# Optimization experiments

Measured on AMD Instinct MI355X. Metric: run time of the kernel, lower is better.

## Reference

```python
import jax, jax.numpy as jnp
import numpy as np

N, IN_DIM, HID = 8192, 256, 128


def _glorot(key, shape):
    lim = float(np.sqrt(6.0 / (shape[0] + shape[1])))
    return jax.random.uniform(key, shape, jnp.float32, -lim, lim)


def setup_inputs() -> dict:
    key = jax.random.key(0)
    ks = jax.random.split(key, 16)
    return {
        "x": jax.random.normal(ks[0], (N, IN_DIM), jnp.float32),
        "XY_Adj": jnp.zeros((N, N), jnp.float32),  # unused: overwritten by Cos_Adj in forward
        "w0": _glorot(ks[1], (IN_DIM, HID)),
        "w1": _glorot(ks[2], (IN_DIM, HID)),
        "Wq1": _glorot(ks[3], (IN_DIM, HID)), "bq1": jnp.zeros((HID,), jnp.float32),
        "Wk1": _glorot(ks[4], (IN_DIM, HID)), "bk1": jnp.zeros((HID,), jnp.float32),
        "Wv1": _glorot(ks[5], (IN_DIM, HID)), "bv1": jnp.zeros((HID,), jnp.float32),
        "Ws1": _glorot(ks[6], (IN_DIM, HID)), "bs1": jnp.zeros((HID,), jnp.float32),
        "Wq4": _glorot(ks[7], (HID, IN_DIM)), "bq4": jnp.zeros((IN_DIM,), jnp.float32),
        "Wk4": _glorot(ks[8], (HID, IN_DIM)), "bk4": jnp.zeros((IN_DIM,), jnp.float32),
        "Wv4": _glorot(ks[9], (HID, IN_DIM)), "bv4": jnp.zeros((IN_DIM,), jnp.float32),
        "Ws4": _glorot(ks[10], (HID, IN_DIM)), "bs4": jnp.zeros((IN_DIM,), jnp.float32),
    }


def _cos_adj(x, w0, w1):
    # Dense cosine-similarity adjacency, as in Cos_Adj.forward
    theta = x @ w0  # [N, HID]
    phi = x @ w1    # [N, HID]
    tn = jnp.linalg.norm(theta, axis=1, keepdims=True)  # [N,1]
    pn = jnp.linalg.norm(phi, axis=1, keepdims=True)    # [N,1]
    return (theta @ phi.T) / (tn @ pn.T + 1e-20)        # [N,N]


def _tconv(h, Wq, bq, Wk, bk, Wv, bv, Ws, bs):
    # PyG TransformerConv (heads=1, root_weight=True) on the fully-connected
    # graph produced by coo_matrix(sim_graph) == dense all-pairs attention.
    q = h @ Wq + bq
    k = h @ Wk + bk
    v = h @ Wv + bv
    scale = 1.0 / np.sqrt(q.shape[-1])
    attn = jax.nn.softmax((q @ k.T) * scale, axis=-1)  # [N,N]
    return attn @ v + (h @ Ws + bs)


def reference(x, XY_Adj, w0, w1,
              Wq1, bq1, Wk1, bk1, Wv1, bv1, Ws1, bs1,
              Wq4, bq4, Wk4, bk4, Wv4, bv4, Ws4, bs4):
    # Adjacency values only define the edge set (all N^2 pairs nonzero for
    # generic inputs); TransformerConv recomputes attention coefficients.
    sim = _cos_adj(x, w0, w1)  # noqa: F841 (edge set = nonzeros = all pairs)
    h1 = jax.nn.elu(_tconv(x, Wq1, bq1, Wk1, bk1, Wv1, bv1, Ws1, bs1))
    out = _tconv(h1, Wq4, bq4, Wk4, bk4, Wv4, bv4, Ws4, bs4)
    return out
```

## Files before the change

### kernel.cpp

```cpp
#include <hip/hip_runtime.h>

#define N_ROWS 8192
#define IN_DIM 256
#define HID 128

typedef __attribute__((ext_vector_type(8))) short bf16x8;
typedef __attribute__((ext_vector_type(4))) float f32x4;

__device__ __forceinline__ unsigned short f2bf(float f) {
    union { float f; unsigned u; } v; v.f = f;
    unsigned r = (v.u + 0x7FFFu + ((v.u >> 16) & 1u)) >> 16;
    return (unsigned short)r;
}

__device__ __forceinline__ unsigned cvt_pk_bf16(float lo, float hi) {
    unsigned r;
    asm("v_cvt_pk_bf16_f32 %0, %1, %2" : "=v"(r) : "v"(lo), "v"(hi));
    return r;
}

__global__ void pack_weights(const float* __restrict__ W0, const float* __restrict__ W1,
                             const float* __restrict__ W2, const float* __restrict__ W3,
                             const float* __restrict__ b0, const float* __restrict__ b1,
                             const float* __restrict__ b2, const float* __restrict__ b3,
                             unsigned short* __restrict__ WT, float* __restrict__ B,
                             int K, int HO)
{
    int NT = 4 * HO;
    int idx = blockIdx.x * blockDim.x + threadIdx.x;
    if (idx < NT * K) {
        int n = idx / K, k = idx - n * K;
        int s = n / HO, sn = n - s * HO;
        const float* W = (s == 0) ? W0 : (s == 1) ? W1 : (s == 2) ? W2 : W3;
        WT[idx] = f2bf(W[k * HO + sn]);
    }
    if (idx < NT) {
        int s = idx / HO, sn = idx - s * HO;
        const float* b = (s == 0) ? b0 : (s == 1) ? b1 : (s == 2) ? b2 : b3;
        B[idx] = b[sn];
    }
}

__global__ void cast_x(const float* __restrict__ in, unsigned short* __restrict__ out, int n) {
    int i = blockIdx.x * blockDim.x + threadIdx.x;
    if (i < n) out[i] = f2bf(in[i]);
}

__global__ void transpose_bf16(const unsigned short* __restrict__ in,
                               unsigned short* __restrict__ out, int R, int C)
{
    __shared__ unsigned short t[32][33];
    const int tx = threadIdx.x, ty = threadIdx.y;
    const int r0 = blockIdx.y * 32, c0 = blockIdx.x * 32;
    #pragma unroll
    for (int j = 0; j < 32; j += 8)
        t[ty + j][tx] = in[(size_t)(r0 + ty + j) * C + c0 + tx];
    __syncthreads();
    #pragma unroll
    for (int j = 0; j < 32; j += 8)
        out[(size_t)(c0 + ty + j) * R + r0 + tx] = t[tx][ty + j];
}

template<int K>
__global__ __launch_bounds__(256) void proj_gemm(
    const unsigned short* __restrict__ A, const unsigned short* __restrict__ WT,
    const float* __restrict__ bias,
    unsigned short* __restrict__ qo, unsigned short* __restrict__ ko,
    unsigned short* __restrict__ vo, float* __restrict__ skip,
    int NT, float qScale)
{
    const int lane = threadIdx.x & 63;
    const int wid = (blockIdx.x * blockDim.x + threadIdx.x) >> 6;
    const int nStrips = NT / 64;
    const int mTile = wid / nStrips;
    const int nBase = (wid - mTile * nStrips) * 64;
    const int l15 = lane & 15, lg = lane >> 4;
    const int HO = NT >> 2;

    f32x4 acc[4];
    #pragma unroll
    for (int c = 0; c < 4; ++c) acc[c] = f32x4{0.f, 0.f, 0.f, 0.f};

    const unsigned short* Ap = A + (size_t)(mTile * 16 + l15) * K + lg * 8;
    #pragma unroll
    for (int t = 0; t < K / 32; ++t) {
        bf16x8 a = *(const bf16x8*)(Ap + t * 32);
        #pragma unroll
        for (int c = 0; c < 4; ++c) {
            bf16x8 b = *(const bf16x8*)(WT + (size_t)(nBase + c * 16 + l15) * K + t * 32 + lg * 8);
            acc[c] = __builtin_amdgcn_mfma_f32_16x16x32_bf16(a, b, acc[c], 0, 0, 0);
        }
    }
    #pragma unroll
    for (int c = 0; c < 4; ++c) {
        int col = nBase + c * 16 + l15;
        int sec = col / HO, sc = col - sec * HO;
        float bv = bias[col];
        #pragma unroll
        for (int r = 0; r < 4; ++r) {
            int mrow = mTile * 16 + lg * 4 + r;
            float val = acc[c][r] + bv;
            size_t o = (size_t)mrow * HO + sc;
            if (sec == 0) qo[o] = f2bf(val * qScale);
            else if (sec == 1) ko[o] = f2bf(val);
            else if (sec == 2) vo[o] = f2bf(val);
            else skip[o] = val;
        }
    }
}

template<int D, int KB>
__global__ __launch_bounds__(512) void attn_partial(
    const unsigned short* __restrict__ Qm,
    const unsigned short* __restrict__ Km,
    const unsigned short* __restrict__ VTg,
    float* __restrict__ accOut, float* __restrict__ mOut, float* __restrict__ lOut,
    int chunkLen)
{
    constexpr int TPB = 512;
    constexpr int LK = D + 8;
    constexpr int LV = KB + 8;
    constexpr int DT = D / 16;
    constexpr int CT = KB / 16;
    constexpr int KS = KB / 32;
    static_assert(KB * D / 8 / TPB == 2, "two K staging int4s per thread");
    static_assert(D * KB / 8 / TPB == 2, "two V staging int4s per thread");
    __shared__ __align__(16) unsigned short Kl[KB * LK];
    __shared__ __align__(16) unsigned short VTl[D * LV];

    const int tid = threadIdx.x;
    const int lane = tid & 63;
    const int w = tid >> 6;
    const int l15 = lane & 15, lg = lane >> 4;
    const int qrow = blockIdx.x * 128 + w * 16;
    const int kStart = blockIdx.y * chunkLen;
    const size_t NN = N_ROWS;

    const int kr0 = tid / (D / 8), kc0 = tid - kr0 * (D / 8);
    const int kr1 = (tid + TPB) / (D / 8), kc1 = (tid + TPB) - kr1 * (D / 8);
    const int kg0 = kr0 * D + kc0 * 8, kl0 = kr0 * LK + kc0 * 8;
    const int kg1 = kr1 * D + kc1 * 8, kl1 = kr1 * LK + kc1 * 8;
    const int vr0 = tid / (KB / 8), vc0 = tid - vr0 * (KB / 8);
    const int vr1 = (tid + TPB) / (KB / 8), vc1 = (tid + TPB) - vr1 * (KB / 8);
    const int vg0 = vr0 * (int)NN + vc0 * 8, vl0 = vr0 * LV + vc0 * 8;
    const int vg1 = vr1 * (int)NN + vc1 * 8, vl1 = vr1 * LV + vc1 * 8;

    bf16x8 qf[D / 32];
    #pragma unroll
    for (int t = 0; t < D / 32; ++t)
        qf[t] = *(const bf16x8*)(Qm + (size_t)(qrow + l15) * D + t * 32 + lg * 8);

    f32x4 acc[DT];
    #pragma unroll
    for (int dt = 0; dt < DT; ++dt) acc[dt] = f32x4{0.f, 0.f, 0.f, 0.f};
    float mReg = -__builtin_inff();
    float lReg = 0.f;

    const int nt = chunkLen / KB;
    const unsigned short* Kp = Km + (size_t)kStart * D;
    const unsigned short* Vp = VTg + kStart;
    int4 pk0 = *(const int4*)(Kp + kg0);
    int4 pk1 = *(const int4*)(Kp + kg1);
    int4 pv0 = *(const int4*)(Vp + vg0);
    int4 pv1 = *(const int4*)(Vp + vg1);

    for (int t = 0; t < nt; ++t) {
        __syncthreads();
        *(int4*)(&Kl[kl0]) = pk0;
        *(int4*)(&Kl[kl1]) = pk1;
        *(int4*)(&VTl[vl0]) = pv0;
        *(int4*)(&VTl[vl1]) = pv1;
        __syncthreads();
        if (t + 1 < nt) {
            const unsigned short* KpN = Kp + (size_t)(t + 1) * KB * D;
            const unsigned short* VpN = Vp + (t + 1) * KB;
            pk0 = *(const int4*)(KpN + kg0);
            pk1 = *(const int4*)(KpN + kg1);
            pv0 = *(const int4*)(VpN + vg0);
            pv1 = *(const int4*)(VpN + vg1);
        }
        f32x4 sT[CT];
        __builtin_amdgcn_s_setprio(1);
        #pragma unroll
        for (int c = 0; c < CT; ++c) {
            sT[c] = f32x4{0.f, 0.f, 0.f, 0.f};
            #pragma unroll
            for (int tt = 0; tt < D / 32; ++tt) {
                bf16x8 kf = *(const bf16x8*)(&Kl[(c * 16 + l15) * LK + tt * 32 + lg * 8]);
                sT[c] = __builtin_amdgcn_mfma_f32_16x16x32_bf16(kf, qf[tt], sT[c], 0, 0, 0);
            }
        }
        __builtin_amdgcn_s_setprio(0);
        float pmax = sT[0][0];
        #pragma unroll
        for (int c = 0; c < CT; ++c)
            #pragma unroll
            for (int r = 0; r < 4; ++r) pmax = fmaxf(pmax, sT[c][r]);
        bool need = pmax > mReg + 8.f;
        if (__any(need)) {
            float v = pmax;
            v = fmaxf(v, __shfl_xor(v, 16));
            v = fmaxf(v, __shfl_xor(v, 32));
            float mN = fmaxf(mReg, v);
            float al = exp2f(mReg - mN);
            mReg = mN;
            lReg *= al;
            #pragma unroll
            for (int dt = 0; dt < DT; ++dt) acc[dt] *= al;
        }
        unsigned Wp[CT][2];
        float lsum = 0.f;
        #pragma unroll
        for (int c = 0; c < CT; ++c) {
            float p0 = exp2f(sT[c][0] - mReg);
            float p1 = exp2f(sT[c][1] - mReg);
            float p2 = exp2f(sT[c][2] - mReg);
            float p3 = exp2f(sT[c][3] - mReg);
            lsum += (p0 + p1) + (p2 + p3);
            Wp[c][0] = cvt_pk_bf16(p0, p1);
            Wp[c][1] = cvt_pk_bf16(p2, p3);
        }
        lReg += lsum;
        #pragma unroll
        for (int ks = 0; ks < KS; ++ks) {
            unsigned x0 = Wp[2 * ks][0], x1 = Wp[2 * ks][1];
            unsigned x2 = Wp[2 * ks + 1][0], x3 = Wp[2 * ks + 1][1];
            const bool g1 = (lg & 2) != 0, g0 = (lg & 1) != 0;
            unsigned s0 = g1 ? x0 : x2, s1 = g1 ? x1 : x3;
            unsigned r0 = __shfl_xor(s0, 32), r1 = __shfl_xor(s1, 32);
            unsigned k0 = g1 ? x2 : x0, k1 = g1 ? x3 : x1;
            unsigned t0 = (g0 != g1) ? k0 : r0, t1 = (g0 != g1) ? k1 : r1;
            unsigned q0 = __shfl_xor(t0, 16), q1 = __shfl_xor(t1, 16);
            union { unsigned u[4]; bf16x8 v; } pb;
            pb.u[0] = g0 ? q0 : (g1 ? r0 : k0);
            pb.u[1] = g0 ? q1 : (g1 ? r1 : k1);
            pb.u[2] = g0 ? (g1 ? k0 : r0) : q0;
            pb.u[3] = g0 ? (g1 ? k1 : r1) : q1;
            __builtin_amdgcn_s_setprio(1);
            #pragma unroll
            for (int dt = 0; dt < DT; ++dt) {
                bf16x8 va = *(const bf16x8*)(&VTl[(dt * 16 + l15) * LV + ks * 32 + lg * 8]);
                acc[dt] = __builtin_amdgcn_mfma_f32_16x16x32_bf16(va, pb.v, acc[dt], 0, 0, 0);
            }
            __builtin_amdgcn_s_setprio(0);
        }
    }

    lReg += __shfl_xor(lReg, 16);
    lReg += __shfl_xor(lReg, 32);

    float* accRow = accOut + ((size_t)blockIdx.y * NN + qrow + l15) * D + lg * 4;
    #pragma unroll
    for (int dt = 0; dt < DT; ++dt)
        *(f32x4*)(accRow + dt * 16) = acc[dt];
    if (lg == 0) {
        mOut[blockIdx.y * NN + qrow + l15] = mReg;
        lOut[blockIdx.y * NN + qrow + l15] = lReg;
    }
}

template<int D, bool ELU>
__global__ void combine_kernel(const float* __restrict__ acc, const float* __restrict__ mArr,
                               const float* __restrict__ lArr, const float* __restrict__ skip,
                               float* __restrict__ outF, unsigned short* __restrict__ outB,
                               int CH)
{
    const int row = blockIdx.x;
    const int d = threadIdx.x;
    const size_t NN = N_ROWS;
    float mStar = -__builtin_inff();
    for (int c = 0; c < CH; ++c) mStar = fmaxf(mStar, mArr[c * NN + row]);
    float denom = 0.f, val = 0.f;
    for (int c = 0; c < CH; ++c) {
        float wgt = exp2f(mArr[c * NN + row] - mStar);
        denom += wgt * lArr[c * NN + row];
        val += wgt * acc[((size_t)c * NN + row) * D + d];
    }
    float v = val / denom + skip[(size_t)row * D + d];
    if (ELU) {
        v = (v > 0.f) ? v : expm1f(v);
        outB[(size_t)row * D + d] = f2bf(v);
    } else {
        outF[(size_t)row * D + d] = v;
    }
}

extern "C" void kernel_launch(void* const* d_in, const int* in_sizes, int n_in,
                              void* d_out, int out_size, void* d_ws, size_t ws_size,
                              hipStream_t stream)
{
    (void)in_sizes; (void)n_in; (void)out_size;
    const float* x   = (const float*)d_in[0];
    const float* Wq1 = (const float*)d_in[4];
    const float* bq1 = (const float*)d_in[5];
    const float* Wk1 = (const float*)d_in[6];
    const float* bk1 = (const float*)d_in[7];
    const float* Wv1 = (const float*)d_in[8];
    const float* bv1 = (const float*)d_in[9];
    const float* Ws1 = (const float*)d_in[10];
    const float* bs1 = (const float*)d_in[11];
    const float* Wq4 = (const float*)d_in[12];
    const float* bq4 = (const float*)d_in[13];
    const float* Wk4 = (const float*)d_in[14];
    const float* bk4 = (const float*)d_in[15];
    const float* Wv4 = (const float*)d_in[16];
    const float* bv4 = (const float*)d_in[17];
    const float* Ws4 = (const float*)d_in[18];
    const float* bs4 = (const float*)d_in[19];
    float* out = (float*)d_out;

    const int N = N_ROWS;
    size_t off = 0;
    auto alloc = [&](size_t bytes) -> void* {
        void* p = (char*)d_ws + off;
        off = (off + bytes + 255) & ~(size_t)255;
        return p;
    };
    unsigned short* xb  = (unsigned short*)alloc((size_t)N * IN_DIM * 2);
    unsigned short* WT1 = (unsigned short*)alloc((size_t)512 * 256 * 2);
    float* B1           = (float*)alloc(512 * 4);
    unsigned short* WT4 = (unsigned short*)alloc((size_t)1024 * 128 * 2);
    float* B4           = (float*)alloc(1024 * 4);
    unsigned short* q1  = (unsigned short*)alloc((size_t)N * HID * 2);
    unsigned short* k1  = (unsigned short*)alloc((size_t)N * HID * 2);
    unsigned short* v1  = (unsigned short*)alloc((size_t)N * HID * 2);
    unsigned short* VT1g= (unsigned short*)alloc((size_t)HID * N * 2);
    float* skip1        = (float*)alloc((size_t)N * HID * 4);
    unsigned short* h1  = (unsigned short*)alloc((size_t)N * HID * 2);
    unsigned short* q4  = (unsigned short*)alloc((size_t)N * IN_DIM * 2);
    unsigned short* k4  = (unsigned short*)alloc((size_t)N * IN_DIM * 2);
    unsigned short* v4  = (unsigned short*)alloc((size_t)N * IN_DIM * 2);
    unsigned short* VT4g= (unsigned short*)alloc((size_t)IN_DIM * N * 2);
    float* skip4        = (float*)alloc((size_t)N * IN_DIM * 4);

    size_t fixedEnd = off;
    size_t perCH = (size_t)N * 4 * 4 + (size_t)N * HID * 4 + (size_t)N * IN_DIM * 4 + 4096;
    int CH = 8;
    while (CH > 1 && fixedEnd + (size_t)CH * perCH > ws_size) CH >>= 1;

    float* m1   = (float*)alloc((size_t)CH * N * 4);
    float* l1   = (float*)alloc((size_t)CH * N * 4);
    float* m2   = (float*)alloc((size_t)CH * N * 4);
    float* l2   = (float*)alloc((size_t)CH * N * 4);
    float* acc1 = (float*)alloc((size_t)CH * N * HID * 4);
    float* acc2 = (float*)alloc((size_t)CH * N * IN_DIM * 4);
    if (off > ws_size && CH == 1) acc2 = out;

    const float LOG2E = 1.4426950408889634f;
    const float qs1 = 0.088388347648318447f * LOG2E;
    const float qs2 = 0.0625f * LOG2E;

    pack_weights<<<dim3((512 * 256 + 255) / 256), dim3(256), 0, stream>>>(
        Wq1, Wk1, Wv1, Ws1, bq1, bk1, bv1, bs1, WT1, B1, 256, 128);
    pack_weights<<<dim3((1024 * 128 + 255) / 256), dim3(256), 0, stream>>>(
        Wq4, Wk4, Wv4, Ws4, bq4, bk4, bv4, bs4, WT4, B4, 128, 256);
    cast_x<<<dim3((N * IN_DIM + 255) / 256), dim3(256), 0, stream>>>(x, xb, N * IN_DIM);

    proj_gemm<256><<<dim3((N / 16) * (512 / 64) / 4), dim3(256), 0, stream>>>(
        xb, WT1, B1, q1, k1, v1, skip1, 512, qs1);
    transpose_bf16<<<dim3(HID / 32, N / 32), dim3(32, 8), 0, stream>>>(v1, VT1g, N, HID);
    attn_partial<128, 64><<<dim3(N / 128, CH), dim3(512), 0, stream>>>(
        q1, k1, VT1g, acc1, m1, l1, N / CH);
    combine_kernel<128, true><<<dim3(N), dim3(128), 0, stream>>>(
        acc1, m1, l1, skip1, (float*)nullptr, h1, CH);

    proj_gemm<128><<<dim3((N / 16) * (1024 / 64) / 4), dim3(256), 0, stream>>>(
        h1, WT4, B4, q4, k4, v4, skip4, 1024, qs2);
    transpose_bf16<<<dim3(IN_DIM / 32, N / 32), dim3(32, 8), 0, stream>>>(v4, VT4g, N, IN_DIM);
    attn_partial<256, 32><<<dim3(N / 128, CH), dim3(512), 0, stream>>>(
        q4, k4, VT4g, acc2, m2, l2, N / CH);
    combine_kernel<256, false><<<dim3(N), dim3(256), 0, stream>>>(
        acc2, m2, l2, skip4, out, (unsigned short*)nullptr, CH);
}
```

Baseline: 277.9 us.

## Process two 16-row query tiles per wave in attention to reuse K/V LDS fragments

Each wave now handles 32 query rows (two 16-row MFMA tiles) instead of 16. Every K and V fragment read from LDS is reused across both query tiles, which halves LDS reads and K/V global staging per query row. The grid is halved to match. In exchange, register pressure roughly doubles for the accumulators, which matters most for D=256, and there are fewer blocks to fill the GPU, especially if CH is small.

```diff
diff --git a/kernel.cpp b/kernel.cpp
--- a/kernel.cpp
+++ b/kernel.cpp
@@ -109,7 +109,7 @@
     }
 }
 
-template<int D, int KB>
+template<int D, int KB, int Q2>
 __global__ __launch_bounds__(512) void attn_partial(
     const unsigned short* __restrict__ Qm,
     const unsigned short* __restrict__ Km,
@@ -123,6 +123,7 @@
     constexpr int DT = D / 16;
     constexpr int CT = KB / 16;
     constexpr int KS = KB / 32;
+    constexpr int QW = 16 * Q2;
     static_assert(KB * D / 8 / TPB == 2, "two K staging int4s per thread");
     static_assert(D * KB / 8 / TPB == 2, "two V staging int4s per thread");
     __shared__ __align__(16) unsigned short Kl[KB * LK];
@@ -132,7 +133,7 @@
     const int lane = tid & 63;
     const int w = tid >> 6;
     const int l15 = lane & 15, lg = lane >> 4;
-    const int qrow = blockIdx.x * 128 + w * 16;
+    const int qrow = blockIdx.x * (8 * QW) + w * QW;
     const int kStart = blockIdx.y * chunkLen;
     const size_t NN = N_ROWS;
 
@@ -145,16 +146,22 @@
     const int vg0 = vr0 * (int)NN + vc0 * 8, vl0 = vr0 * LV + vc0 * 8;
     const int vg1 = vr1 * (int)NN + vc1 * 8, vl1 = vr1 * LV + vc1 * 8;
 
-    bf16x8 qf[D / 32];
-    #pragma unroll
-    for (int t = 0; t < D / 32; ++t)
-        qf[t] = *(const bf16x8*)(Qm + (size_t)(qrow + l15) * D + t * 32 + lg * 8);
-
-    f32x4 acc[DT];
-    #pragma unroll
-    for (int dt = 0; dt < DT; ++dt) acc[dt] = f32x4{0.f, 0.f, 0.f, 0.f};
-    float mReg = -__builtin_inff();
-    float lReg = 0.f;
+    bf16x8 qf[Q2][D / 32];
+    #pragma unroll
+    for (int m = 0; m < Q2; ++m)
+        #pragma unroll
+        for (int t = 0; t < D / 32; ++t)
+            qf[m][t] = *(const bf16x8*)(Qm + (size_t)(qrow + m * 16 + l15) * D + t * 32 + lg * 8);
+
+    f32x4 acc[Q2][DT];
+    float mReg[Q2], lReg[Q2];
+    #pragma unroll
+    for (int m = 0; m < Q2; ++m) {
+        #pragma unroll
+        for (int dt = 0; dt < DT; ++dt) acc[m][dt] = f32x4{0.f, 0.f, 0.f, 0.f};
+        mReg[m] = -__builtin_inff();
+        lReg[m] = 0.f;
+    }
 
     const int nt = chunkLen / KB;
     const unsigned short* Kp = Km + (size_t)kStart * D;
@@ -179,83 +186,108 @@
             pv0 = *(const int4*)(VpN + vg0);
             pv1 = *(const int4*)(VpN + vg1);
         }
-        f32x4 sT[CT];
+        f32x4 sT[Q2][CT];
         __builtin_amdgcn_s_setprio(1);
         #pragma unroll
         for (int c = 0; c < CT; ++c) {
-            sT[c] = f32x4{0.f, 0.f, 0.f, 0.f};
+            #pragma unroll
+            for (int m = 0; m < Q2; ++m) sT[m][c] = f32x4{0.f, 0.f, 0.f, 0.f};
             #pragma unroll
             for (int tt = 0; tt < D / 32; ++tt) {
                 bf16x8 kf = *(const bf16x8*)(&Kl[(c * 16 + l15) * LK + tt * 32 + lg * 8]);
-                sT[c] = __builtin_amdgcn_mfma_f32_16x16x32_bf16(kf, qf[tt], sT[c], 0, 0, 0);
+                #pragma unroll
+                for (int m = 0; m < Q2; ++m)
+                    sT[m][c] = __builtin_amdgcn_mfma_f32_16x16x32_bf16(kf, qf[m][tt], sT[m][c], 0, 0, 0);
             }
         }
         __builtin_amdgcn_s_setprio(0);
-        float pmax = sT[0][0];
-        #pragma unroll
-        for (int c = 0; c < CT; ++c)
-            #pragma unroll
-            for (int r = 0; r < 4; ++r) pmax = fmaxf(pmax, sT[c][r]);
-        bool need = pmax > mReg + 8.f;
+        float pmax[Q2];
+        bool need = false;
+        #pragma unroll
+        for (int m = 0; m < Q2; ++m) {
+            float v = sT[m][0][0];
+            #pragma unroll
+            for (int c = 0; c < CT; ++c)
+                #pragma unroll
+                for (int r = 0; r < 4; ++r) v = fmaxf(v, sT[m][c][r]);
+            pmax[m] = v;
+            need = need || (v > mReg[m] + 8.f);
+        }
         if (__any(need)) {
-            float v = pmax;
-            v = fmaxf(v, __shfl_xor(v, 16));
-            v = fmaxf(v, __shfl_xor(v, 32));
-            float mN = fmaxf(mReg, v);
-            float al = exp2f(mReg - mN);
-            mReg = mN;
-            lReg *= al;
-            #pragma unroll
-            for (int dt = 0; dt < DT; ++dt) acc[dt] *= al;
-        }
-        unsigned Wp[CT][2];
-        float lsum = 0.f;
-        #pragma unroll
-        for (int c = 0; c < CT; ++c) {
-            float p0 = exp2f(sT[c][0] - mReg);
-            float p1 = exp2f(sT[c][1] - mReg);
-            float p2 = exp2f(sT[c][2] - mReg);
-            float p3 = exp2f(sT[c][3] - mReg);
-            lsum += (p0 + p1) + (p2 + p3);
-            Wp[c][0] = cvt_pk_bf16(p0, p1);
-            Wp[c][1] = cvt_pk_bf16(p2, p3);
-        }
-        lReg += lsum;
+            #pragma unroll
+            for (int m = 0; m < Q2; ++m) {
+                float v = pmax[m];
+                v = fmaxf(v, __shfl_xor(v, 16));
+                v = fmaxf(v, __shfl_xor(v, 32));
+                float mN = fmaxf(mReg[m], v);
+                float al = exp2f(mReg[m] - mN);
+                mReg[m] = mN;
+                lReg[m] *= al;
+                #pragma unroll
+                for (int dt = 0; dt < DT; ++dt) acc[m][dt] *= al;
+            }
+        }
+        unsigned Wp[Q2][CT][2];
+        #pragma unroll
+        for (int m = 0; m < Q2; ++m) {
+            float lsum = 0.f;
+            #pragma unroll
+            for (int c = 0; c < CT; ++c) {
+                float p0 = exp2f(sT[m][c][0] - mReg[m]);
+                float p1 = exp2f(sT[m][c][1] - mReg[m]);
+                float p2 = exp2f(sT[m][c][2] - mReg[m]);
+                float p3 = exp2f(sT[m][c][3] - mReg[m]);
+                lsum += (p0 + p1) + (p2 + p3);
+                Wp[m][c][0] = cvt_pk_bf16(p0, p1);
+                Wp[m][c][1] = cvt_pk_bf16(p2, p3);
+            }
+            lReg[m] += lsum;
+        }
         #pragma unroll
         for (int ks = 0; ks < KS; ++ks) {
-            unsigned x0 = Wp[2 * ks][0], x1 = Wp[2 * ks][1];
-            unsigned x2 = Wp[2 * ks + 1][0], x3 = Wp[2 * ks + 1][1];
-            const bool g1 = (lg & 2) != 0, g0 = (lg & 1) != 0;
-            unsigned s0 = g1 ? x0 : x2, s1 = g1 ? x1 : x3;
-            unsigned r0 = __shfl_xor(s0, 32), r1 = __shfl_xor(s1, 32);
-            unsigned k0 = g1 ? x2 : x0, k1 = g1 ? x3 : x1;
-            unsigned t0 = (g0 != g1) ? k0 : r0, t1 = (g0 != g1) ? k1 : r1;
-            unsigned q0 = __shfl_xor(t0, 16), q1 = __shfl_xor(t1, 16);
-            union { unsigned u[4]; bf16x8 v; } pb;
-            pb.u[0] = g0 ? q0 : (g1 ? r0 : k0);
-            pb.u[1] = g0 ? q1 : (g1 ? r1 : k1);
-            pb.u[2] = g0 ? (g1 ? k0 : r0) : q0;
-            pb.u[3] = g0 ? (g1 ? k1 : r1) : q1;
+            bf16x8 pbv[Q2];
+            #pragma unroll
+            for (int m = 0; m < Q2; ++m) {
+                unsigned x0 = Wp[m][2 * ks][0], x1 = Wp[m][2 * ks][1];
+                unsigned x2 = Wp[m][2 * ks + 1][0], x3 = Wp[m][2 * ks + 1][1];
+                const bool g1 = (lg & 2) != 0, g0 = (lg & 1) != 0;
+                unsigned s0 = g1 ? x0 : x2, s1 = g1 ? x1 : x3;
+                unsigned r0 = __shfl_xor(s0, 32), r1 = __shfl_xor(s1, 32);
+                unsigned k0 = g1 ? x2 : x0, k1 = g1 ? x3 : x1;
+                unsigned t0 = (g0 != g1) ? k0 : r0, t1 = (g0 != g1) ? k1 : r1;
+                unsigned q0 = __shfl_xor(t0, 16), q1 = __shfl_xor(t1, 16);
+                union { unsigned u[4]; bf16x8 v; } pb;
+                pb.u[0] = g0 ? q0 : (g1 ? r0 : k0);
+                pb.u[1] = g0 ? q1 : (g1 ? r1 : k1);
+                pb.u[2] = g0 ? (g1 ? k0 : r0) : q0;
+                pb.u[3] = g0 ? (g1 ? k1 : r1) : q1;
+                pbv[m] = pb.v;
+            }
             __builtin_amdgcn_s_setprio(1);
             #pragma unroll
             for (int dt = 0; dt < DT; ++dt) {
                 bf16x8 va = *(const bf16x8*)(&VTl[(dt * 16 + l15) * LV + ks * 32 + lg * 8]);
-                acc[dt] = __builtin_amdgcn_mfma_f32_16x16x32_bf16(va, pb.v, acc[dt], 0, 0, 0);
+                #pragma unroll
+                for (int m = 0; m < Q2; ++m)
+                    acc[m][dt] = __builtin_amdgcn_mfma_f32_16x16x32_bf16(va, pbv[m], acc[m][dt], 0, 0, 0);
             }
             __builtin_amdgcn_s_setprio(0);
         }
     }
 
-    lReg += __shfl_xor(lReg, 16);
-    lReg += __shfl_xor(lReg, 32);
-
-    float* accRow = accOut + ((size_t)blockIdx.y * NN + qrow + l15) * D + lg * 4;
-    #pragma unroll
-    for (int dt = 0; dt < DT; ++dt)
-        *(f32x4*)(accRow + dt * 16) = acc[dt];
-    if (lg == 0) {
-        mOut[blockIdx.y * NN + qrow + l15] = mReg;
-        lOut[blockIdx.y * NN + qrow + l15] = lReg;
+    #pragma unroll
+    for (int m = 0; m < Q2; ++m) {
+        float lv = lReg[m];
+        lv += __shfl_xor(lv, 16);
+        lv += __shfl_xor(lv, 32);
+        float* accRow = accOut + ((size_t)blockIdx.y * NN + qrow + m * 16 + l15) * D + lg * 4;
+        #pragma unroll
+        for (int dt = 0; dt < DT; ++dt)
+            *(f32x4*)(accRow + dt * 16) = acc[m][dt];
+        if (lg == 0) {
+            mOut[blockIdx.y * NN + qrow + m * 16 + l15] = mReg[m];
+            lOut[blockIdx.y * NN + qrow + m * 16 + l15] = lv;
+        }
     }
 }
 
@@ -359,7 +391,7 @@
     proj_gemm<256><<<dim3((N / 16) * (512 / 64) / 4), dim3(256), 0, stream>>>(
         xb, WT1, B1, q1, k1, v1, skip1, 512, qs1);
     transpose_bf16<<<dim3(HID / 32, N / 32), dim3(32, 8), 0, stream>>>(v1, VT1g, N, HID);
-    attn_partial<128, 64><<<dim3(N / 128, CH), dim3(512), 0, stream>>>(
+    attn_partial<128, 64, 2><<<dim3(N / 256, CH), dim3(512), 0, stream>>>(
         q1, k1, VT1g, acc1, m1, l1, N / CH);
     combine_kernel<128, true><<<dim3(N), dim3(128), 0, stream>>>(
         acc1, m1, l1, skip1, (float*)nullptr, h1, CH);
@@ -367,7 +399,7 @@
     proj_gemm<128><<<dim3((N / 16) * (1024 / 64) / 4), dim3(256), 0, stream>>>(
         h1, WT4, B4, q4, k4, v4, skip4, 1024, qs2);
     transpose_bf16<<<dim3(IN_DIM / 32, N / 32), dim3(32, 8), 0, stream>>>(v4, VT4g, N, IN_DIM);
-    attn_partial<256, 32><<<dim3(N / 128, CH), dim3(512), 0, stream>>>(
+    attn_partial<256, 32, 2><<<dim3(N / 256, CH), dim3(512), 0, stream>>>(
         q4, k4, VT4g, acc2, m2, l2, N / CH);
     combine_kernel<256, false><<<dim3(N), dim3(256), 0, stream>>>(
         acc2, m2, l2, skip4, out, (unsigned short*)nullptr, CH);
```

Result: faster. 271.0 us, median of 2 (-2.5%).
